# Performance work log

Measured on AMD Instinct MI355X. Metric: run time of the kernel, lower is better.

Reference implementation:

```python
import jax, jax.numpy as jnp
import numpy as np

B, T, A_DIM, Z_DIM, K = 128, 80, 32, 64, 16


def setup_inputs() -> dict:
    key = jax.random.key(0)
    k1, k2, k3, k4 = jax.random.split(key, 4)
    obs = jax.random.normal(k1, (B, T, A_DIM), jnp.float32)
    alpha_logits = jax.random.normal(k2, (B, T, K), jnp.float32)
    # torch init: A = eye(z) repeated K times; small noise keeps 80-step recursion stable
    A_K = jnp.eye(Z_DIM, dtype=jnp.float32)[None] + 0.005 * jax.random.normal(k3, (K, Z_DIM, Z_DIM), jnp.float32)
    # torch init: C = 0.05 * randn
    C_K = 0.05 * jax.random.normal(k4, (K, A_DIM, Z_DIM), jnp.float32)
    return {"obs": obs, "alpha_logits": alpha_logits, "A_K": A_K, "C_K": C_K}


def _kalman(obs, A, C):
    # obs [B,T,a], A [B,T,z,z], C [B,T,a,z]
    Bq, Tq, a_dim = obs.shape
    z_dim = A.shape[-1]
    dt = obs.dtype
    Q = 0.08 * jnp.eye(z_dim, dtype=dt)
    R = 0.03 * jnp.eye(a_dim, dtype=dt)
    I = jnp.eye(z_dim, dtype=dt)

    obs_t = jnp.swapaxes(obs, 0, 1)          # [T,B,a]
    A_t = jnp.swapaxes(A, 0, 1)              # [T,B,z,z]
    C_t = jnp.swapaxes(C, 0, 1)              # [T,B,a,z]
    A_next = jnp.concatenate([A_t[1:], A_t[-1:]], axis=0)  # A[t+1]; last unused

    mu0 = jnp.zeros((Bq, z_dim), dt)
    sig0 = jnp.broadcast_to(20.0 * I, (Bq, z_dim, z_dim))

    def filt_step(carry, inp):
        mu_p, sig_p, mu_prev = carry
        At, Anx, Ct, y = inp
        CtT = jnp.swapaxes(Ct, -1, -2)
        S = Ct @ sig_p @ CtT + R                       # [B,a,a]
        Kg = sig_p @ CtT @ jnp.linalg.inv(S)            # [B,z,a]
        Amu = jnp.einsum('bij,bj->bi', At, mu_prev)     # A_t mu_{t-1}
        err = y - jnp.einsum('bij,bj->bi', Ct, Amu)
        mu_f = Amu + jnp.einsum('bij,bj->bi', Kg, err)
        sig_f = (I - Kg @ Ct) @ sig_p
        mu_pn = jnp.einsum('bij,bj->bi', Anx, mu_f)     # prediction with A_{t+1}
        sig_pn = Anx @ sig_f @ jnp.swapaxes(Anx, -1, -2) + Q
        return (mu_pn, sig_pn, mu_f), (mu_f, sig_f, mu_p, sig_p)

    _, (mu_f, sig_f, mu_p, sig_p) = jax.lax.scan(
        filt_step, (mu0, sig0, mu0), (A_t, A_next, C_t, obs_t))

    def smooth_step(carry, inp):
        mu_s, sig_s = carry
        mf, sf, Anx, mpn, spn = inp
        J = sf @ jnp.swapaxes(Anx, -1, -2) @ jnp.linalg.inv(spn)
        mu = mf + jnp.einsum('bij,bj->bi', J, mu_s - mpn)
        sig = sf + J @ (sig_s - spn) @ jnp.swapaxes(J, -1, -2)
        return (mu, sig), (mu, sig)

    init = (mu_f[-1], sig_f[-1])
    _, (mu_sm, sig_sm) = jax.lax.scan(
        smooth_step, init,
        (mu_f[:-1], sig_f[:-1], A_t[1:], mu_p[1:], sig_p[1:]),
        reverse=True)
    mu_sm = jnp.concatenate([mu_sm, mu_f[-1:]], axis=0)
    sig_sm = jnp.concatenate([sig_sm, sig_f[-1:]], axis=0)
    return jnp.swapaxes(mu_sm, 0, 1), jnp.swapaxes(sig_sm, 0, 1)  # [B,T,z], [B,T,z,z]


def reference(obs, alpha_logits, A_K, C_K):
    w = jax.nn.softmax(alpha_logits, axis=-1)                # [B,T,K]
    A = jnp.einsum('btk,kij->btij', w, A_K)                  # [B,T,z,z]
    C = jnp.einsum('btk,kij->btij', w, C_K)                  # [B,T,a,z]
    return _kalman(obs, A, C)
```

## Files before the change

### kernel.cpp

```cpp
#include <hip/hip_runtime.h>

#define B_ 128
#define T_ 80
#define AD 32
#define ZD 64
#define KD 16
#define S8 68
#define SC 36

__device__ __forceinline__ float4 ld4(const float* p) { return *(const float4*)p; }
__device__ __forceinline__ void st4f(float* p, float4 v) { *(float4*)p = v; }

__device__ __forceinline__ float4 comb4(float4 c, float4 x0, float4 x1, float4 x2, float4 x3) {
    return make_float4(c.x*x0.x + c.y*x1.x + c.z*x2.x + c.w*x3.x,
                       c.x*x0.y + c.y*x1.y + c.z*x2.y + c.w*x3.y,
                       c.x*x0.z + c.y*x1.z + c.z*x2.z + c.w*x3.z,
                       c.x*x0.w + c.y*x1.w + c.z*x2.w + c.w*x3.w);
}

__device__ __forceinline__ void pinv4(float4 q0, float4 q1, float4 q2, float4 q3,
                                      float4& pi0, float4& pi1, float4& pi2, float4& pi3)
{
    const float ra = 1.0f / (q0.x*q1.y - q0.y*q1.x);
    const float ai00 =  q1.y*ra, ai01 = -q0.y*ra, ai10 = -q1.x*ra, ai11 = q0.x*ra;
    const float ca00 = q2.x*ai00 + q2.y*ai10, ca01 = q2.x*ai01 + q2.y*ai11;
    const float ca10 = q3.x*ai00 + q3.y*ai10, ca11 = q3.x*ai01 + q3.y*ai11;
    const float s00 = q2.z - (ca00*q0.z + ca01*q1.z), s01 = q2.w - (ca00*q0.w + ca01*q1.w);
    const float s10 = q3.z - (ca10*q0.z + ca11*q1.z), s11 = q3.w - (ca10*q0.w + ca11*q1.w);
    const float rs = 1.0f / (s00*s11 - s01*s10);
    const float si00 = s11*rs, si01 = -s01*rs, si10 = -s10*rs, si11 = s00*rs;
    const float ab00 = ai00*q0.z + ai01*q1.z, ab01 = ai00*q0.w + ai01*q1.w;
    const float ab10 = ai10*q0.z + ai11*q1.z, ab11 = ai10*q0.w + ai11*q1.w;
    const float t00 = ab00*si00 + ab01*si10, t01 = ab00*si01 + ab01*si11;
    const float t10 = ab10*si00 + ab11*si10, t11 = ab10*si01 + ab11*si11;
    const float tl00 = ai00 + (t00*ca00 + t01*ca10), tl01 = ai01 + (t00*ca01 + t01*ca11);
    const float tl10 = ai10 + (t10*ca00 + t11*ca10), tl11 = ai11 + (t10*ca01 + t11*ca11);
    const float bl00 = -(si00*ca00 + si01*ca10), bl01 = -(si00*ca01 + si01*ca11);
    const float bl10 = -(si10*ca00 + si11*ca10), bl11 = -(si10*ca01 + si11*ca11);
    pi0 = make_float4(tl00, tl01, -t00, -t01);
    pi1 = make_float4(tl10, tl11, -t10, -t11);
    pi2 = make_float4(bl00, bl01, si00, si01);
    pi3 = make_float4(bl10, bl11, si10, si11);
}

template<int KL, int AS, int BS, bool ATRANS>
__device__ __forceinline__ void mm64(const float* __restrict__ Pa, const float* __restrict__ Qb,
                                     float acc[2][4], int r2, int c4)
{
#pragma unroll 8
    for (int k = 0; k < KL; k++) {
        float aA, aB;
        if (ATRANS) { aA = Pa[k * AS + r2];   aB = Pa[k * AS + r2 + 1]; }
        else        { aA = Pa[r2 * AS + k];   aB = Pa[(r2 + 1) * AS + k]; }
        const float4 bv = ld4(&Qb[k * BS + c4]);
        acc[0][0] += aA * bv.x; acc[0][1] += aA * bv.y; acc[0][2] += aA * bv.z; acc[0][3] += aA * bv.w;
        acc[1][0] += aB * bv.x; acc[1][1] += aB * bv.y; acc[1][2] += aB * bv.z; acc[1][3] += aB * bv.w;
    }
}

__global__ __launch_bounds__(512, 2)
void kvae_kernel(const float* __restrict__ obs, const float* __restrict__ logits,
                 const float* __restrict__ AK, const float* __restrict__ CK,
                 float* __restrict__ out)
{
    __shared__ __align__(16) float W[T_ * KD];
    __shared__ __align__(16) float Am[ZD * S8];
    __shared__ __align__(16) float At[ZD * S8];
    __shared__ __align__(16) float SP[ZD * S8];
    __shared__ __align__(16) float SF[ZD * S8];
    __shared__ __align__(16) float Mm[ZD * S8];
    __shared__ __align__(16) float Pool[9984];
    __shared__ __align__(16) float pvL[512];
    __shared__ __align__(16) float pvR[512];
    __shared__ __align__(16) float fbb[512];
    __shared__ __align__(16) float pvE[8];
    __shared__ __align__(16) float y_s[32];
    __shared__ __align__(16) float errv[32];
    __shared__ __align__(16) float uev[32];
    __shared__ __align__(16) float mup[64];
    __shared__ __align__(16) float muf[64];
    __shared__ __align__(16) float mus[64];
    __shared__ __align__(16) float mpn[64];
    __shared__ __align__(16) float dv[64];

    float* T1 = Pool;
    float* CM = Pool + 2176;
    float* CT = Pool + 4352;
    float* U_ = Pool + 6656;
    float* S_ = Pool + 8832;
    float* Xb = Pool;
    float* SG = Pool + 4352;

    const int tid = threadIdx.x;
    const int b   = blockIdx.x;

    const int r16 = tid >> 4;
    const int cg  = tid & 15;
    const int c4  = cg << 2;
    const int c2  = cg << 1;
    const int r2  = r16 << 1;
    const int gi  = tid >> 3;
    const int gs  = tid & 7;

    const float* obs_b = obs    + (size_t)b * T_ * AD;
    const float* lg_b  = logits + (size_t)b * T_ * KD;
    float* omu = out + (size_t)b * T_ * ZD;
    float* osg = out + (size_t)B_ * T_ * ZD + (size_t)b * T_ * ZD * ZD;
    const float4* AK4 = (const float4*)AK;
    const float4* CK4 = (const float4*)CK;

    auto mixA = [&](int tt) {
#pragma unroll
        for (int rr = 0; rr < 2; rr++) {
            const int r = r2 + rr;
            float4 a = make_float4(0.f, 0.f, 0.f, 0.f);
#pragma unroll
            for (int k = 0; k < KD; k++) {
                const float wk = W[tt * KD + k];
                const float4 v = AK4[k * 1024 + r * 16 + cg];
                a.x += wk * v.x; a.y += wk * v.y; a.z += wk * v.z; a.w += wk * v.w;
            }
            st4f(&Am[r * S8 + c4], a);
            At[(c4 + 0) * S8 + r] = a.x; At[(c4 + 1) * S8 + r] = a.y;
            At[(c4 + 2) * S8 + r] = a.z; At[(c4 + 3) * S8 + r] = a.w;
        }
    };
    auto mixC = [&](int tt) {
        float4 a = make_float4(0.f, 0.f, 0.f, 0.f);
#pragma unroll
        for (int k = 0; k < KD; k++) {
            const float wk = W[tt * KD + k];
            const float4 v = CK4[k * 512 + r16 * 16 + cg];
            a.x += wk * v.x; a.y += wk * v.y; a.z += wk * v.z; a.w += wk * v.w;
        }
        st4f(&CM[r16 * S8 + c4], a);
        CT[(c4 + 0) * SC + r16] = a.x; CT[(c4 + 1) * SC + r16] = a.y;
        CT[(c4 + 2) * SC + r16] = a.z; CT[(c4 + 3) * SC + r16] = a.w;
    };

    if (tid < T_) {
        float l[KD]; float mx = -1e30f;
#pragma unroll
        for (int k = 0; k < KD; k++) { l[k] = lg_b[tid * KD + k]; mx = fmaxf(mx, l[k]); }
        float s = 0.f;
#pragma unroll
        for (int k = 0; k < KD; k++) { l[k] = expf(l[k] - mx); s += l[k]; }
        const float inv = 1.0f / s;
#pragma unroll
        for (int k = 0; k < KD; k++) W[tid * KD + k] = l[k] * inv;
    }
#pragma unroll
    for (int rr = 0; rr < 2; rr++) {
        const int r = r2 + rr;
#pragma unroll
        for (int j = 0; j < 4; j++) SP[r * S8 + c4 + j] = (r == c4 + j) ? 20.0f : 0.0f;
    }
    if (tid < ZD) mup[tid] = 0.0f;
    __syncthreads();

    for (int t = 0; t < T_; t++) {
        if (t < T_ - 1) mixA(t + 1);
        mixC(t);
        if (tid < AD) y_s[tid] = obs_b[t * AD + tid];
        __syncthreads();

        {
            float a0 = 0, a1 = 0, a2 = 0, a3 = 0;
            const float* pa = CM + r16 * S8;
#pragma unroll 8
            for (int k = 0; k < ZD; k++) {
                const float a = pa[k];
                const float4 bv = ld4(&SP[k * S8 + c4]);
                a0 += a * bv.x; a1 += a * bv.y; a2 += a * bv.z; a3 += a * bv.w;
            }
            T1[r16 * S8 + c4 + 0] = a0; T1[r16 * S8 + c4 + 1] = a1;
            T1[r16 * S8 + c4 + 2] = a2; T1[r16 * S8 + c4 + 3] = a3;
        }
        __syncthreads();

        {
            float a0 = 0, a1 = 0;
            const float* pa = T1 + r16 * S8;
#pragma unroll 8
            for (int k = 0; k < ZD; k++) {
                const float a = pa[k];
                const float2 bv = *(const float2*)&CT[k * SC + c2];
                a0 += a * bv.x; a1 += a * bv.y;
            }
            if (r16 == c2)     a0 += 0.03f;
            if (r16 == c2 + 1) a1 += 0.03f;
            S_[r16 * SC + c2] = a0; S_[r16 * SC + c2 + 1] = a1;
        }
        if (tid < AD) {
            float s = 0.f;
#pragma unroll
            for (int k4 = 0; k4 < ZD; k4 += 4) {
                const float4 cm = ld4(&CM[tid * S8 + k4]);
                const float4 mu = ld4(&mup[k4]);
                s += cm.x*mu.x + cm.y*mu.y + cm.z*mu.z + cm.w*mu.w;
            }
            errv[tid] = y_s[tid] - s;
        }
        __syncthreads();

        {
            const int hi = r16, hs = cg;
            float4 aL = make_float4(0, 0, 0, 0);
            float4 aR = ld4(&T1[hi * S8 + hs * 4]);
            float e = 0.f;
            if (hs < 8) aL = ld4(&S_[hi * SC + hs * 4]);
            if (hs == 15) e = errv[hi];
            if (hi < 4) {
                if (hs < 8) st4f(&pvL[hi * 32 + hs * 4], aL);
                st4f(&pvR[hi * 64 + hs * 4], aR);
                if (hs == 15) pvE[hi] = e;
            }
            if (hs == 0) st4f(&fbb[hi * 4], aL);
            __syncthreads();

#pragma unroll 2
            for (int j = 0; j < 8; ++j) {
                const int par = j & 1, nb = par ^ 1;
                const bool isp = (hi >> 2) == j;
                const float4 f  = ld4(&fbb[par * 128 + hi * 4]);
                const float4 q0 = ld4(&fbb[par * 128 + (4 * j + 0) * 4]);
                const float4 q1 = ld4(&fbb[par * 128 + (4 * j + 1) * 4]);
                const float4 q2 = ld4(&fbb[par * 128 + (4 * j + 2) * 4]);
                const float4 q3 = ld4(&fbb[par * 128 + (4 * j + 3) * 4]);
                float4 pi0, pi1, pi2, pi3;
                pinv4(q0, q1, q2, q3, pi0, pi1, pi2, pi3);
                const int rr = hi & 3;
                const float4 coef = isp ? (rr == 0 ? pi0 : rr == 1 ? pi1 : rr == 2 ? pi2 : pi3)
                                        : comb4(f, pi0, pi1, pi2, pi3);
                {
                    const float4 x0 = ld4(&pvR[par * 256 + 0 * 64 + hs * 4]);
                    const float4 x1 = ld4(&pvR[par * 256 + 1 * 64 + hs * 4]);
                    const float4 x2 = ld4(&pvR[par * 256 + 2 * 64 + hs * 4]);
                    const float4 x3 = ld4(&pvR[par * 256 + 3 * 64 + hs * 4]);
                    const float4 c = comb4(coef, x0, x1, x2, x3);
                    if (isp) aR = c;
                    else { aR.x -= c.x; aR.y -= c.y; aR.z -= c.z; aR.w -= c.w; }
                }
                if (hs < 8) {
                    const float4 x0 = ld4(&pvL[par * 128 + 0 * 32 + hs * 4]);
                    const float4 x1 = ld4(&pvL[par * 128 + 1 * 32 + hs * 4]);
                    const float4 x2 = ld4(&pvL[par * 128 + 2 * 32 + hs * 4]);
                    const float4 x3 = ld4(&pvL[par * 128 + 3 * 32 + hs * 4]);
                    const float4 c = comb4(coef, x0, x1, x2, x3);
                    if (isp) aL = c;
                    else { aL.x -= c.x; aL.y -= c.y; aL.z -= c.z; aL.w -= c.w; }
                }
                if (hs == 15) {
                    const float e0 = pvE[par * 4 + 0], e1 = pvE[par * 4 + 1];
                    const float e2 = pvE[par * 4 + 2], e3 = pvE[par * 4 + 3];
                    const float ce = coef.x * e0 + coef.y * e1 + coef.z * e2 + coef.w * e3;
                    if (isp) e = ce; else e -= ce;
                }
                if (j < 7) {
                    if ((hi >> 2) == j + 1) {
                        if (hs < 8) st4f(&pvL[nb * 128 + (hi & 3) * 32 + hs * 4], aL);
                        st4f(&pvR[nb * 256 + (hi & 3) * 64 + hs * 4], aR);
                        if (hs == 15) pvE[nb * 4 + (hi & 3)] = e;
                    }
                    if (hs == j + 1) st4f(&fbb[nb * 128 + hi * 4], aL);
                }
                __syncthreads();
            }
            st4f(&U_[hi * S8 + hs * 4], aR);
            if (hs == 15) uev[hi] = e;
        }
        __syncthreads();

        {
            float acc[2][4] = {};
            mm64<AD, S8, S8, true>(T1, U_, acc, r2, c4);
            float* og = osg + (size_t)t * ZD * ZD;
#pragma unroll
            for (int rr = 0; rr < 2; rr++) {
                const int r = r2 + rr;
                const float4 sp = ld4(&SP[r * S8 + c4]);
                const float4 v = make_float4(sp.x - acc[rr][0], sp.y - acc[rr][1],
                                             sp.z - acc[rr][2], sp.w - acc[rr][3]);
                st4f(&SF[r * S8 + c4], v);
                *(float4*)(og + r * ZD + c4) = v;
            }
        }
        if (tid < ZD) {
            float s = 0.f;
#pragma unroll
            for (int k = 0; k < AD; k++) s += T1[k * S8 + tid] * uev[k];
            const float v = mup[tid] + s;
            muf[tid] = v;
            omu[t * ZD + tid] = v;
        }
        __syncthreads();

        if (t < T_ - 1) {
            {
                float acc[2][4] = {};
                mm64<ZD, S8, S8, false>(Am, SF, acc, r2, c4);
#pragma unroll
                for (int rr = 0; rr < 2; rr++)
                    st4f(&Mm[(r2 + rr) * S8 + c4],
                         make_float4(acc[rr][0], acc[rr][1], acc[rr][2], acc[rr][3]));
            }
            __syncthreads();
            {
                float acc[2][4] = {};
                mm64<ZD, S8, S8, false>(Mm, At, acc, r2, c4);
#pragma unroll
                for (int rr = 0; rr < 2; rr++) {
                    const int r = r2 + rr;
#pragma unroll
                    for (int j = 0; j < 4; j++)
                        SP[r * S8 + c4 + j] = acc[rr][j] + ((r == c4 + j) ? 0.08f : 0.0f);
                }
            }
            if (tid >= 448) {
                const int i = tid - 448;
                float s = 0.f;
                const float* pa = Am + i * S8;
#pragma unroll 8
                for (int k = 0; k < ZD; k++) s += pa[k] * muf[k];
                mup[i] = s;
            }
            __syncthreads();
        }
    }

#pragma unroll
    for (int rr = 0; rr < 2; rr++)
        st4f(&SG[(r2 + rr) * S8 + c4], ld4(&SF[(r2 + rr) * S8 + c4]));
    if (tid < ZD) mus[tid] = muf[tid];
    __syncthreads();

    for (int t = T_ - 2; t >= 0; t--) {
        mixA(t + 1);
        {
            const float4* og4 = (const float4*)(osg + (size_t)t * ZD * ZD);
#pragma unroll
            for (int rr = 0; rr < 2; rr++)
                st4f(&SF[(r2 + rr) * S8 + c4], og4[(r2 + rr) * 16 + cg]);
        }
        if (tid >= 448) muf[tid - 448] = omu[t * ZD + (tid - 448)];
        __syncthreads();

        {
            float acc[2][4] = {};
            mm64<ZD, S8, S8, false>(Am, SF, acc, r2, c4);
#pragma unroll
            for (int rr = 0; rr < 2; rr++)
                st4f(&Mm[(r2 + rr) * S8 + c4],
                     make_float4(acc[rr][0], acc[rr][1], acc[rr][2], acc[rr][3]));
        }
        if (tid >= 448) {
            const int i = tid - 448;
            float s = 0.f;
            const float* pa = Am + i * S8;
#pragma unroll 8
            for (int k = 0; k < ZD; k++) s += pa[k] * muf[k];
            mpn[i] = s;
        }
        __syncthreads();

        {
            float acc[2][4] = {};
            mm64<ZD, S8, S8, false>(Mm, At, acc, r2, c4);
#pragma unroll
            for (int rr = 0; rr < 2; rr++) {
                const int r = r2 + rr;
#pragma unroll
                for (int j = 0; j < 4; j++)
                    SP[r * S8 + c4 + j] = acc[rr][j] + ((r == c4 + j) ? 0.08f : 0.0f);
            }
        }
        if (tid >= 448) { const int i = tid - 448; dv[i] = mus[i] - mpn[i]; }
        __syncthreads();

        {
            float4 aL0 = ld4(&SP[gi * S8 + gs * 8]);
            float4 aL1 = ld4(&SP[gi * S8 + gs * 8 + 4]);
            float4 aR0 = ld4(&Mm[gi * S8 + gs * 8]);
            float4 aR1 = ld4(&Mm[gi * S8 + gs * 8 + 4]);
            if (gi < 4) {
                st4f(&pvL[gi * 64 + gs * 8], aL0); st4f(&pvL[gi * 64 + gs * 8 + 4], aL1);
                st4f(&pvR[gi * 64 + gs * 8], aR0); st4f(&pvR[gi * 64 + gs * 8 + 4], aR1);
            }
            if (gs == 0) st4f(&fbb[gi * 4], aL0);
            __syncthreads();

#pragma unroll 2
            for (int j = 0; j < 16; ++j) {
                const int par = j & 1, nb = par ^ 1;
                const bool isp = (gi >> 2) == j;
                const float4 f  = ld4(&fbb[par * 256 + gi * 4]);
                const float4 q0 = ld4(&fbb[par * 256 + (4 * j + 0) * 4]);
                const float4 q1 = ld4(&fbb[par * 256 + (4 * j + 1) * 4]);
                const float4 q2 = ld4(&fbb[par * 256 + (4 * j + 2) * 4]);
                const float4 q3 = ld4(&fbb[par * 256 + (4 * j + 3) * 4]);
                float4 pi0, pi1, pi2, pi3;
                pinv4(q0, q1, q2, q3, pi0, pi1, pi2, pi3);
                const int rr = gi & 3;
                const float4 coef = isp ? (rr == 0 ? pi0 : rr == 1 ? pi1 : rr == 2 ? pi2 : pi3)
                                        : comb4(f, pi0, pi1, pi2, pi3);
                {
                    const float4 x0 = ld4(&pvL[par * 256 + 0 * 64 + gs * 8]);
                    const float4 x1 = ld4(&pvL[par * 256 + 1 * 64 + gs * 8]);
                    const float4 x2 = ld4(&pvL[par * 256 + 2 * 64 + gs * 8]);
                    const float4 x3 = ld4(&pvL[par * 256 + 3 * 64 + gs * 8]);
                    const float4 c = comb4(coef, x0, x1, x2, x3);
                    if (isp) aL0 = c;
                    else { aL0.x -= c.x; aL0.y -= c.y; aL0.z -= c.z; aL0.w -= c.w; }
                }
                {
                    const float4 x0 = ld4(&pvL[par * 256 + 0 * 64 + gs * 8 + 4]);
                    const float4 x1 = ld4(&pvL[par * 256 + 1 * 64 + gs * 8 + 4]);
                    const float4 x2 = ld4(&pvL[par * 256 + 2 * 64 + gs * 8 + 4]);
                    const float4 x3 = ld4(&pvL[par * 256 + 3 * 64 + gs * 8 + 4]);
                    const float4 c = comb4(coef, x0, x1, x2, x3);
                    if (isp) aL1 = c;
                    else { aL1.x -= c.x; aL1.y -= c.y; aL1.z -= c.z; aL1.w -= c.w; }
                }
                {
                    const float4 x0 = ld4(&pvR[par * 256 + 0 * 64 + gs * 8]);
                    const float4 x1 = ld4(&pvR[par * 256 + 1 * 64 + gs * 8]);
                    const float4 x2 = ld4(&pvR[par * 256 + 2 * 64 + gs * 8]);
                    const float4 x3 = ld4(&pvR[par * 256 + 3 * 64 + gs * 8]);
                    const float4 c = comb4(coef, x0, x1, x2, x3);
                    if (isp) aR0 = c;
                    else { aR0.x -= c.x; aR0.y -= c.y; aR0.z -= c.z; aR0.w -= c.w; }
                }
                {
                    const float4 x0 = ld4(&pvR[par * 256 + 0 * 64 + gs * 8 + 4]);
                    const float4 x1 = ld4(&pvR[par * 256 + 1 * 64 + gs * 8 + 4]);
                    const float4 x2 = ld4(&pvR[par * 256 + 2 * 64 + gs * 8 + 4]);
                    const float4 x3 = ld4(&pvR[par * 256 + 3 * 64 + gs * 8 + 4]);
                    const float4 c = comb4(coef, x0, x1, x2, x3);
                    if (isp) aR1 = c;
                    else { aR1.x -= c.x; aR1.y -= c.y; aR1.z -= c.z; aR1.w -= c.w; }
                }
                if (j < 15) {
                    if ((gi >> 2) == j + 1) {
                        const int rn = gi & 3;
                        st4f(&pvL[nb * 256 + rn * 64 + gs * 8], aL0);
                        st4f(&pvL[nb * 256 + rn * 64 + gs * 8 + 4], aL1);
                        st4f(&pvR[nb * 256 + rn * 64 + gs * 8], aR0);
                        st4f(&pvR[nb * 256 + rn * 64 + gs * 8 + 4], aR1);
                    }
                    if (gs == ((j + 1) >> 1))
                        st4f(&fbb[nb * 256 + gi * 4], ((j + 1) & 1) ? aL1 : aL0);
                }
                __syncthreads();
            }
            st4f(&Xb[gi * S8 + gs * 8], aR0);
            st4f(&Xb[gi * S8 + gs * 8 + 4], aR1);
        }
        __syncthreads();

        {
            float acc[2][4] = {};
            mm64<ZD, S8, S8, false>(SG, Xb, acc, r2, c4);
#pragma unroll
            for (int rr = 0; rr < 2; rr++) {
                const int r = r2 + rr;
                const float4 m = ld4(&Mm[r * S8 + c4]);
                SP[r * S8 + c4 + 0] = acc[rr][0] - m.x;
                SP[r * S8 + c4 + 1] = acc[rr][1] - m.y;
                SP[r * S8 + c4 + 2] = acc[rr][2] - m.z;
                SP[r * S8 + c4 + 3] = acc[rr][3] - m.w;
            }
        }
        __syncthreads();

        {
            float acc[2][4] = {};
            mm64<ZD, S8, S8, true>(Xb, SP, acc, r2, c4);
            float* og = osg + (size_t)t * ZD * ZD;
#pragma unroll
            for (int rr = 0; rr < 2; rr++) {
                const int r = r2 + rr;
                const float4 sf = ld4(&SF[r * S8 + c4]);
                const float4 v = make_float4(sf.x + acc[rr][0], sf.y + acc[rr][1],
                                             sf.z + acc[rr][2], sf.w + acc[rr][3]);
                st4f(&SG[r * S8 + c4], v);
                *(float4*)(og + r * ZD + c4) = v;
            }
        }
        if (tid < ZD) {
            float s = 0.f;
#pragma unroll 8
            for (int k = 0; k < ZD; k++) s += Xb[k * S8 + tid] * dv[k];
            const float v = muf[tid] + s;
            mus[tid] = v;
            omu[t * ZD + tid] = v;
        }
        __syncthreads();
    }
}

extern "C" void kernel_launch(void* const* d_in, const int* in_sizes, int n_in,
                              void* d_out, int out_size, void* d_ws, size_t ws_size,
                              hipStream_t stream) {
    const float* obs = (const float*)d_in[0];
    const float* lg  = (const float*)d_in[1];
    const float* AK  = (const float*)d_in[2];
    const float* CK  = (const float*)d_in[3];
    (void)d_ws; (void)ws_size; (void)in_sizes; (void)n_in; (void)out_size;
    kvae_kernel<<<dim3(B_), dim3(512), 0, stream>>>(obs, lg, AK, CK, (float*)d_out);
}
```

Baseline: 3.609 ms.

## Double block size to 1024 threads with one output row-quad per thread

Launches 1024 threads per batch element instead of 512 and remaps every 64x64 matmul so each thread computes one row of four outputs rather than two. The 32x32 innovation covariance and the block Gauss-Jordan eliminations are redistributed across the wider block, and eliminations now skip columns that are already reduced. The aim is to cut the serial per-thread work inside this latency-bound recursion, since only 128 blocks exist on a large GPU. The cost is more threads waiting at each barrier, fewer registers per thread, and an extra barrier where the S computation was split out.

```diff
diff --git a/kernel.cpp b/kernel.cpp
--- a/kernel.cpp
+++ b/kernel.cpp
@@ -10,7 +10,9 @@
 
 __device__ __forceinline__ float4 ld4(const float* p) { return *(const float4*)p; }
 __device__ __forceinline__ void st4f(float* p, float4 v) { *(float4*)p = v; }
-
+__device__ __forceinline__ float4 sub4(float4 a, float4 b) {
+    return make_float4(a.x - b.x, a.y - b.y, a.z - b.z, a.w - b.w);
+}
 __device__ __forceinline__ float4 comb4(float4 c, float4 x0, float4 x1, float4 x2, float4 x3) {
     return make_float4(c.x*x0.x + c.y*x1.x + c.z*x2.x + c.w*x3.x,
                        c.x*x0.y + c.y*x1.y + c.z*x2.y + c.w*x3.y,
@@ -44,21 +46,20 @@
 }
 
 template<int KL, int AS, int BS, bool ATRANS>
-__device__ __forceinline__ void mm64(const float* __restrict__ Pa, const float* __restrict__ Qb,
-                                     float acc[2][4], int r2, int c4)
+__device__ __forceinline__ float4 mm14(const float* __restrict__ Pa, const float* __restrict__ Qb,
+                                       int r, int c4)
 {
+    float a0 = 0.f, a1 = 0.f, a2 = 0.f, a3 = 0.f;
 #pragma unroll 8
     for (int k = 0; k < KL; k++) {
-        float aA, aB;
-        if (ATRANS) { aA = Pa[k * AS + r2];   aB = Pa[k * AS + r2 + 1]; }
-        else        { aA = Pa[r2 * AS + k];   aB = Pa[(r2 + 1) * AS + k]; }
+        const float a = ATRANS ? Pa[k * AS + r] : Pa[r * AS + k];
         const float4 bv = ld4(&Qb[k * BS + c4]);
-        acc[0][0] += aA * bv.x; acc[0][1] += aA * bv.y; acc[0][2] += aA * bv.z; acc[0][3] += aA * bv.w;
-        acc[1][0] += aB * bv.x; acc[1][1] += aB * bv.y; acc[1][2] += aB * bv.z; acc[1][3] += aB * bv.w;
+        a0 += a * bv.x; a1 += a * bv.y; a2 += a * bv.z; a3 += a * bv.w;
     }
-}
-
-__global__ __launch_bounds__(512, 2)
+    return make_float4(a0, a1, a2, a3);
+}
+
+__global__ __launch_bounds__(1024, 4)
 void kvae_kernel(const float* __restrict__ obs, const float* __restrict__ logits,
                  const float* __restrict__ AK, const float* __restrict__ CK,
                  float* __restrict__ out)
@@ -94,13 +95,9 @@
     const int tid = threadIdx.x;
     const int b   = blockIdx.x;
 
-    const int r16 = tid >> 4;
+    const int rw  = tid >> 4;
     const int cg  = tid & 15;
     const int c4  = cg << 2;
-    const int c2  = cg << 1;
-    const int r2  = r16 << 1;
-    const int gi  = tid >> 3;
-    const int gs  = tid & 7;
 
     const float* obs_b = obs    + (size_t)b * T_ * AD;
     const float* lg_b  = logits + (size_t)b * T_ * KD;
@@ -110,32 +107,29 @@
     const float4* CK4 = (const float4*)CK;
 
     auto mixA = [&](int tt) {
-#pragma unroll
-        for (int rr = 0; rr < 2; rr++) {
-            const int r = r2 + rr;
-            float4 a = make_float4(0.f, 0.f, 0.f, 0.f);
-#pragma unroll
-            for (int k = 0; k < KD; k++) {
-                const float wk = W[tt * KD + k];
-                const float4 v = AK4[k * 1024 + r * 16 + cg];
-                a.x += wk * v.x; a.y += wk * v.y; a.z += wk * v.z; a.w += wk * v.w;
-            }
-            st4f(&Am[r * S8 + c4], a);
-            At[(c4 + 0) * S8 + r] = a.x; At[(c4 + 1) * S8 + r] = a.y;
-            At[(c4 + 2) * S8 + r] = a.z; At[(c4 + 3) * S8 + r] = a.w;
-        }
+        float4 a = make_float4(0.f, 0.f, 0.f, 0.f);
+#pragma unroll
+        for (int k = 0; k < KD; k++) {
+            const float wk = W[tt * KD + k];
+            const float4 v = AK4[k * 1024 + rw * 16 + cg];
+            a.x += wk * v.x; a.y += wk * v.y; a.z += wk * v.z; a.w += wk * v.w;
+        }
+        st4f(&Am[rw * S8 + c4], a);
+        At[(c4 + 0) * S8 + rw] = a.x; At[(c4 + 1) * S8 + rw] = a.y;
+        At[(c4 + 2) * S8 + rw] = a.z; At[(c4 + 3) * S8 + rw] = a.w;
     };
     auto mixC = [&](int tt) {
+        const int r = tid >> 4;
         float4 a = make_float4(0.f, 0.f, 0.f, 0.f);
 #pragma unroll
         for (int k = 0; k < KD; k++) {
             const float wk = W[tt * KD + k];
-            const float4 v = CK4[k * 512 + r16 * 16 + cg];
+            const float4 v = CK4[k * 512 + r * 16 + cg];
             a.x += wk * v.x; a.y += wk * v.y; a.z += wk * v.z; a.w += wk * v.w;
         }
-        st4f(&CM[r16 * S8 + c4], a);
-        CT[(c4 + 0) * SC + r16] = a.x; CT[(c4 + 1) * SC + r16] = a.y;
-        CT[(c4 + 2) * SC + r16] = a.z; CT[(c4 + 3) * SC + r16] = a.w;
+        st4f(&CM[r * S8 + c4], a);
+        CT[(c4 + 0) * SC + r] = a.x; CT[(c4 + 1) * SC + r] = a.y;
+        CT[(c4 + 2) * SC + r] = a.z; CT[(c4 + 3) * SC + r] = a.w;
     };
 
     if (tid < T_) {
@@ -150,46 +144,28 @@
         for (int k = 0; k < KD; k++) W[tid * KD + k] = l[k] * inv;
     }
 #pragma unroll
-    for (int rr = 0; rr < 2; rr++) {
-        const int r = r2 + rr;
-#pragma unroll
-        for (int j = 0; j < 4; j++) SP[r * S8 + c4 + j] = (r == c4 + j) ? 20.0f : 0.0f;
-    }
+    for (int j = 0; j < 4; j++) SP[rw * S8 + c4 + j] = (rw == c4 + j) ? 20.0f : 0.0f;
     if (tid < ZD) mup[tid] = 0.0f;
     __syncthreads();
 
     for (int t = 0; t < T_; t++) {
         if (t < T_ - 1) mixA(t + 1);
-        mixC(t);
-        if (tid < AD) y_s[tid] = obs_b[t * AD + tid];
-        __syncthreads();
-
-        {
-            float a0 = 0, a1 = 0, a2 = 0, a3 = 0;
-            const float* pa = CM + r16 * S8;
+        if (tid < 512) mixC(t);
+        if (tid >= 992) y_s[tid - 992] = obs_b[t * AD + (tid - 992)];
+        __syncthreads();
+
+        {
+            const int r = tid >> 5;
+            const int c2 = (tid & 31) << 1;
+            float a0 = 0.f, a1 = 0.f;
+            const float* pa = CM + r * S8;
 #pragma unroll 8
             for (int k = 0; k < ZD; k++) {
                 const float a = pa[k];
-                const float4 bv = ld4(&SP[k * S8 + c4]);
-                a0 += a * bv.x; a1 += a * bv.y; a2 += a * bv.z; a3 += a * bv.w;
-            }
-            T1[r16 * S8 + c4 + 0] = a0; T1[r16 * S8 + c4 + 1] = a1;
-            T1[r16 * S8 + c4 + 2] = a2; T1[r16 * S8 + c4 + 3] = a3;
-        }
-        __syncthreads();
-
-        {
-            float a0 = 0, a1 = 0;
-            const float* pa = T1 + r16 * S8;
-#pragma unroll 8
-            for (int k = 0; k < ZD; k++) {
-                const float a = pa[k];
-                const float2 bv = *(const float2*)&CT[k * SC + c2];
+                const float2 bv = *(const float2*)&SP[k * S8 + c2];
                 a0 += a * bv.x; a1 += a * bv.y;
             }
-            if (r16 == c2)     a0 += 0.03f;
-            if (r16 == c2 + 1) a1 += 0.03f;
-            S_[r16 * SC + c2] = a0; S_[r16 * SC + c2 + 1] = a1;
+            T1[r * S8 + c2] = a0; T1[r * S8 + c2 + 1] = a1;
         }
         if (tid < AD) {
             float s = 0.f;
@@ -204,16 +180,34 @@
         __syncthreads();
 
         {
-            const int hi = r16, hs = cg;
+            const int r = tid >> 5;
+            const int c = tid & 31;
+            float s0 = 0.f, s1 = 0.f;
+            const float* pa = T1 + r * S8;
+            const float* pb = CT + c;
+#pragma unroll 8
+            for (int k = 0; k < ZD; k += 2) {
+                s0 += pa[k] * pb[k * SC];
+                s1 += pa[k + 1] * pb[(k + 1) * SC];
+            }
+            float s = s0 + s1;
+            if (r == c) s += 0.03f;
+            S_[r * SC + c] = s;
+        }
+        __syncthreads();
+
+        {
+            const int hi = tid >> 5, hs = tid & 31;
             float4 aL = make_float4(0, 0, 0, 0);
-            float4 aR = ld4(&T1[hi * S8 + hs * 4]);
+            float4 aR = make_float4(0, 0, 0, 0);
             float e = 0.f;
             if (hs < 8) aL = ld4(&S_[hi * SC + hs * 4]);
-            if (hs == 15) e = errv[hi];
+            else if (hs < 24) aR = ld4(&T1[hi * S8 + (hs - 8) * 4]);
+            else if (hs == 24) e = errv[hi];
             if (hi < 4) {
                 if (hs < 8) st4f(&pvL[hi * 32 + hs * 4], aL);
-                st4f(&pvR[hi * 64 + hs * 4], aR);
-                if (hs == 15) pvE[hi] = e;
+                else if (hs < 24) st4f(&pvR[hi * 64 + (hs - 8) * 4], aR);
+                else if (hs == 24) pvE[hi] = e;
             }
             if (hs == 0) st4f(&fbb[hi * 4], aL);
             __syncthreads();
@@ -221,69 +215,64 @@
 #pragma unroll 2
             for (int j = 0; j < 8; ++j) {
                 const int par = j & 1, nb = par ^ 1;
-                const bool isp = (hi >> 2) == j;
-                const float4 f  = ld4(&fbb[par * 128 + hi * 4]);
-                const float4 q0 = ld4(&fbb[par * 128 + (4 * j + 0) * 4]);
-                const float4 q1 = ld4(&fbb[par * 128 + (4 * j + 1) * 4]);
-                const float4 q2 = ld4(&fbb[par * 128 + (4 * j + 2) * 4]);
-                const float4 q3 = ld4(&fbb[par * 128 + (4 * j + 3) * 4]);
-                float4 pi0, pi1, pi2, pi3;
-                pinv4(q0, q1, q2, q3, pi0, pi1, pi2, pi3);
-                const int rr = hi & 3;
-                const float4 coef = isp ? (rr == 0 ? pi0 : rr == 1 ? pi1 : rr == 2 ? pi2 : pi3)
-                                        : comb4(f, pi0, pi1, pi2, pi3);
-                {
-                    const float4 x0 = ld4(&pvR[par * 256 + 0 * 64 + hs * 4]);
-                    const float4 x1 = ld4(&pvR[par * 256 + 1 * 64 + hs * 4]);
-                    const float4 x2 = ld4(&pvR[par * 256 + 2 * 64 + hs * 4]);
-                    const float4 x3 = ld4(&pvR[par * 256 + 3 * 64 + hs * 4]);
-                    const float4 c = comb4(coef, x0, x1, x2, x3);
-                    if (isp) aR = c;
-                    else { aR.x -= c.x; aR.y -= c.y; aR.z -= c.z; aR.w -= c.w; }
-                }
-                if (hs < 8) {
-                    const float4 x0 = ld4(&pvL[par * 128 + 0 * 32 + hs * 4]);
-                    const float4 x1 = ld4(&pvL[par * 128 + 1 * 32 + hs * 4]);
-                    const float4 x2 = ld4(&pvL[par * 128 + 2 * 32 + hs * 4]);
-                    const float4 x3 = ld4(&pvL[par * 128 + 3 * 32 + hs * 4]);
-                    const float4 c = comb4(coef, x0, x1, x2, x3);
-                    if (isp) aL = c;
-                    else { aL.x -= c.x; aL.y -= c.y; aL.z -= c.z; aL.w -= c.w; }
-                }
-                if (hs == 15) {
-                    const float e0 = pvE[par * 4 + 0], e1 = pvE[par * 4 + 1];
-                    const float e2 = pvE[par * 4 + 2], e3 = pvE[par * 4 + 3];
-                    const float ce = coef.x * e0 + coef.y * e1 + coef.z * e2 + coef.w * e3;
-                    if (isp) e = ce; else e -= ce;
-                }
-                if (j < 7) {
-                    if ((hi >> 2) == j + 1) {
-                        if (hs < 8) st4f(&pvL[nb * 128 + (hi & 3) * 32 + hs * 4], aL);
-                        st4f(&pvR[nb * 256 + (hi & 3) * 64 + hs * 4], aR);
-                        if (hs == 15) pvE[nb * 4 + (hi & 3)] = e;
+                if (hs <= 24) {
+                    const bool isp = (hi >> 2) == j;
+                    const int i4 = hi & 3;
+                    const float4 q0 = ld4(&fbb[par * 128 + (4 * j + 0) * 4]);
+                    const float4 q1 = ld4(&fbb[par * 128 + (4 * j + 1) * 4]);
+                    const float4 q2 = ld4(&fbb[par * 128 + (4 * j + 2) * 4]);
+                    const float4 q3 = ld4(&fbb[par * 128 + (4 * j + 3) * 4]);
+                    float4 pi0, pi1, pi2, pi3;
+                    pinv4(q0, q1, q2, q3, pi0, pi1, pi2, pi3);
+                    float4 coef;
+                    if (isp) coef = (i4 == 0 ? pi0 : i4 == 1 ? pi1 : i4 == 2 ? pi2 : pi3);
+                    else {
+                        const float4 f = ld4(&fbb[par * 128 + hi * 4]);
+                        coef = comb4(f, pi0, pi1, pi2, pi3);
                     }
-                    if (hs == j + 1) st4f(&fbb[nb * 128 + hi * 4], aL);
+                    if (hs < 8) {
+                        if (hs > j - 1) {
+                            const float4 c = comb4(coef,
+                                ld4(&pvL[par * 256 + 0 * 32 + hs * 4]),
+                                ld4(&pvL[par * 256 + 1 * 32 + hs * 4]),
+                                ld4(&pvL[par * 256 + 2 * 32 + hs * 4]),
+                                ld4(&pvL[par * 256 + 3 * 32 + hs * 4]));
+                            if (isp) aL = c; else aL = sub4(aL, c);
+                        }
+                    } else if (hs < 24) {
+                        const float4 c = comb4(coef,
+                            ld4(&pvR[par * 256 + 0 * 64 + (hs - 8) * 4]),
+                            ld4(&pvR[par * 256 + 1 * 64 + (hs - 8) * 4]),
+                            ld4(&pvR[par * 256 + 2 * 64 + (hs - 8) * 4]),
+                            ld4(&pvR[par * 256 + 3 * 64 + (hs - 8) * 4]));
+                        if (isp) aR = c; else aR = sub4(aR, c);
+                    } else {
+                        const float4 ev = ld4(&pvE[par * 4]);
+                        const float ce = coef.x*ev.x + coef.y*ev.y + coef.z*ev.z + coef.w*ev.w;
+                        if (isp) e = ce; else e -= ce;
+                    }
+                    if (j < 7) {
+                        if ((hi >> 2) == j + 1) {
+                            if (hs < 8) { if (hs > j) st4f(&pvL[nb * 256 + i4 * 32 + hs * 4], aL); }
+                            else if (hs < 24) st4f(&pvR[nb * 256 + i4 * 64 + (hs - 8) * 4], aR);
+                            else pvE[nb * 4 + i4] = e;
+                        }
+                        if (hs == j + 1) st4f(&fbb[nb * 128 + hi * 4], aL);
+                    }
                 }
                 __syncthreads();
             }
-            st4f(&U_[hi * S8 + hs * 4], aR);
-            if (hs == 15) uev[hi] = e;
-        }
-        __syncthreads();
-
-        {
-            float acc[2][4] = {};
-            mm64<AD, S8, S8, true>(T1, U_, acc, r2, c4);
-            float* og = osg + (size_t)t * ZD * ZD;
-#pragma unroll
-            for (int rr = 0; rr < 2; rr++) {
-                const int r = r2 + rr;
-                const float4 sp = ld4(&SP[r * S8 + c4]);
-                const float4 v = make_float4(sp.x - acc[rr][0], sp.y - acc[rr][1],
-                                             sp.z - acc[rr][2], sp.w - acc[rr][3]);
-                st4f(&SF[r * S8 + c4], v);
-                *(float4*)(og + r * ZD + c4) = v;
-            }
+            if (hs >= 8 && hs < 24) st4f(&U_[hi * S8 + (hs - 8) * 4], aR);
+            else if (hs == 24) uev[hi] = e;
+        }
+        __syncthreads();
+
+        {
+            const float4 acc = mm14<AD, S8, S8, true>(T1, U_, rw, c4);
+            const float4 sp = ld4(&SP[rw * S8 + c4]);
+            const float4 v = make_float4(sp.x - acc.x, sp.y - acc.y, sp.z - acc.z, sp.w - acc.w);
+            st4f(&SF[rw * S8 + c4], v);
+            *(float4*)(osg + (size_t)t * ZD * ZD + rw * ZD + c4) = v;
         }
         if (tid < ZD) {
             float s = 0.f;
@@ -296,195 +285,136 @@
         __syncthreads();
 
         if (t < T_ - 1) {
-            {
-                float acc[2][4] = {};
-                mm64<ZD, S8, S8, false>(Am, SF, acc, r2, c4);
-#pragma unroll
-                for (int rr = 0; rr < 2; rr++)
-                    st4f(&Mm[(r2 + rr) * S8 + c4],
-                         make_float4(acc[rr][0], acc[rr][1], acc[rr][2], acc[rr][3]));
-            }
+            st4f(&Mm[rw * S8 + c4], mm14<ZD, S8, S8, false>(Am, SF, rw, c4));
             __syncthreads();
             {
-                float acc[2][4] = {};
-                mm64<ZD, S8, S8, false>(Mm, At, acc, r2, c4);
-#pragma unroll
-                for (int rr = 0; rr < 2; rr++) {
-                    const int r = r2 + rr;
-#pragma unroll
-                    for (int j = 0; j < 4; j++)
-                        SP[r * S8 + c4 + j] = acc[rr][j] + ((r == c4 + j) ? 0.08f : 0.0f);
-                }
-            }
-            if (tid >= 448) {
-                const int i = tid - 448;
+                const float4 acc = mm14<ZD, S8, S8, false>(Mm, At, rw, c4);
+                SP[rw * S8 + c4 + 0] = acc.x + ((rw == c4 + 0) ? 0.08f : 0.0f);
+                SP[rw * S8 + c4 + 1] = acc.y + ((rw == c4 + 1) ? 0.08f : 0.0f);
+                SP[rw * S8 + c4 + 2] = acc.z + ((rw == c4 + 2) ? 0.08f : 0.0f);
+                SP[rw * S8 + c4 + 3] = acc.w + ((rw == c4 + 3) ? 0.08f : 0.0f);
+            }
+            if (tid >= 960) {
+                const int i = tid - 960;
                 float s = 0.f;
-                const float* pa = Am + i * S8;
-#pragma unroll 8
-                for (int k = 0; k < ZD; k++) s += pa[k] * muf[k];
+#pragma unroll
+                for (int k4 = 0; k4 < ZD; k4 += 4) {
+                    const float4 am = ld4(&Am[i * S8 + k4]);
+                    const float4 mf = ld4(&muf[k4]);
+                    s += am.x*mf.x + am.y*mf.y + am.z*mf.z + am.w*mf.w;
+                }
                 mup[i] = s;
             }
             __syncthreads();
         }
     }
 
-#pragma unroll
-    for (int rr = 0; rr < 2; rr++)
-        st4f(&SG[(r2 + rr) * S8 + c4], ld4(&SF[(r2 + rr) * S8 + c4]));
+    st4f(&SG[rw * S8 + c4], ld4(&SF[rw * S8 + c4]));
     if (tid < ZD) mus[tid] = muf[tid];
     __syncthreads();
 
     for (int t = T_ - 2; t >= 0; t--) {
         mixA(t + 1);
-        {
-            const float4* og4 = (const float4*)(osg + (size_t)t * ZD * ZD);
-#pragma unroll
-            for (int rr = 0; rr < 2; rr++)
-                st4f(&SF[(r2 + rr) * S8 + c4], og4[(r2 + rr) * 16 + cg]);
-        }
-        if (tid >= 448) muf[tid - 448] = omu[t * ZD + (tid - 448)];
-        __syncthreads();
-
-        {
-            float acc[2][4] = {};
-            mm64<ZD, S8, S8, false>(Am, SF, acc, r2, c4);
-#pragma unroll
-            for (int rr = 0; rr < 2; rr++)
-                st4f(&Mm[(r2 + rr) * S8 + c4],
-                     make_float4(acc[rr][0], acc[rr][1], acc[rr][2], acc[rr][3]));
-        }
-        if (tid >= 448) {
-            const int i = tid - 448;
+        st4f(&SF[rw * S8 + c4],
+             *(const float4*)(osg + (size_t)t * ZD * ZD + rw * ZD + c4));
+        if (tid >= 960) muf[tid - 960] = omu[t * ZD + (tid - 960)];
+        __syncthreads();
+
+        st4f(&Mm[rw * S8 + c4], mm14<ZD, S8, S8, false>(Am, SF, rw, c4));
+        if (tid >= 960) {
+            const int i = tid - 960;
             float s = 0.f;
-            const float* pa = Am + i * S8;
-#pragma unroll 8
-            for (int k = 0; k < ZD; k++) s += pa[k] * muf[k];
+#pragma unroll
+            for (int k4 = 0; k4 < ZD; k4 += 4) {
+                const float4 am = ld4(&Am[i * S8 + k4]);
+                const float4 mf = ld4(&muf[k4]);
+                s += am.x*mf.x + am.y*mf.y + am.z*mf.z + am.w*mf.w;
+            }
             mpn[i] = s;
         }
         __syncthreads();
 
         {
-            float acc[2][4] = {};
-            mm64<ZD, S8, S8, false>(Mm, At, acc, r2, c4);
-#pragma unroll
-            for (int rr = 0; rr < 2; rr++) {
-                const int r = r2 + rr;
-#pragma unroll
-                for (int j = 0; j < 4; j++)
-                    SP[r * S8 + c4 + j] = acc[rr][j] + ((r == c4 + j) ? 0.08f : 0.0f);
-            }
-        }
-        if (tid >= 448) { const int i = tid - 448; dv[i] = mus[i] - mpn[i]; }
-        __syncthreads();
-
-        {
-            float4 aL0 = ld4(&SP[gi * S8 + gs * 8]);
-            float4 aL1 = ld4(&SP[gi * S8 + gs * 8 + 4]);
-            float4 aR0 = ld4(&Mm[gi * S8 + gs * 8]);
-            float4 aR1 = ld4(&Mm[gi * S8 + gs * 8 + 4]);
+            const float4 acc = mm14<ZD, S8, S8, false>(Mm, At, rw, c4);
+            SP[rw * S8 + c4 + 0] = acc.x + ((rw == c4 + 0) ? 0.08f : 0.0f);
+            SP[rw * S8 + c4 + 1] = acc.y + ((rw == c4 + 1) ? 0.08f : 0.0f);
+            SP[rw * S8 + c4 + 2] = acc.z + ((rw == c4 + 2) ? 0.08f : 0.0f);
+            SP[rw * S8 + c4 + 3] = acc.w + ((rw == c4 + 3) ? 0.08f : 0.0f);
+        }
+        if (tid >= 960) { const int i = tid - 960; dv[i] = mus[i] - mpn[i]; }
+        __syncthreads();
+
+        {
+            const int gi = tid >> 4, gs = tid & 15;
+            float4 aL = ld4(&SP[gi * S8 + gs * 4]);
+            float4 aR = ld4(&Mm[gi * S8 + gs * 4]);
             if (gi < 4) {
-                st4f(&pvL[gi * 64 + gs * 8], aL0); st4f(&pvL[gi * 64 + gs * 8 + 4], aL1);
-                st4f(&pvR[gi * 64 + gs * 8], aR0); st4f(&pvR[gi * 64 + gs * 8 + 4], aR1);
-            }
-            if (gs == 0) st4f(&fbb[gi * 4], aL0);
+                st4f(&pvL[gi * 64 + gs * 4], aL);
+                st4f(&pvR[gi * 64 + gs * 4], aR);
+            }
+            if (gs == 0) st4f(&fbb[gi * 4], aL);
             __syncthreads();
 
 #pragma unroll 2
             for (int j = 0; j < 16; ++j) {
                 const int par = j & 1, nb = par ^ 1;
                 const bool isp = (gi >> 2) == j;
-                const float4 f  = ld4(&fbb[par * 256 + gi * 4]);
+                const int i4 = gi & 3;
                 const float4 q0 = ld4(&fbb[par * 256 + (4 * j + 0) * 4]);
                 const float4 q1 = ld4(&fbb[par * 256 + (4 * j + 1) * 4]);
                 const float4 q2 = ld4(&fbb[par * 256 + (4 * j + 2) * 4]);
                 const float4 q3 = ld4(&fbb[par * 256 + (4 * j + 3) * 4]);
                 float4 pi0, pi1, pi2, pi3;
                 pinv4(q0, q1, q2, q3, pi0, pi1, pi2, pi3);
-                const int rr = gi & 3;
-                const float4 coef = isp ? (rr == 0 ? pi0 : rr == 1 ? pi1 : rr == 2 ? pi2 : pi3)
-                                        : comb4(f, pi0, pi1, pi2, pi3);
+                float4 coef;
+                if (isp) coef = (i4 == 0 ? pi0 : i4 == 1 ? pi1 : i4 == 2 ? pi2 : pi3);
+                else {
+                    const float4 f = ld4(&fbb[par * 256 + gi * 4]);
+                    coef = comb4(f, pi0, pi1, pi2, pi3);
+                }
                 {
-                    const float4 x0 = ld4(&pvL[par * 256 + 0 * 64 + gs * 8]);
-                    const float4 x1 = ld4(&pvL[par * 256 + 1 * 64 + gs * 8]);
-                    const float4 x2 = ld4(&pvL[par * 256 + 2 * 64 + gs * 8]);
-                    const float4 x3 = ld4(&pvL[par * 256 + 3 * 64 + gs * 8]);
-                    const float4 c = comb4(coef, x0, x1, x2, x3);
-                    if (isp) aL0 = c;
-                    else { aL0.x -= c.x; aL0.y -= c.y; aL0.z -= c.z; aL0.w -= c.w; }
-                }
-                {
-                    const float4 x0 = ld4(&pvL[par * 256 + 0 * 64 + gs * 8 + 4]);
-                    const float4 x1 = ld4(&pvL[par * 256 + 1 * 64 + gs * 8 + 4]);
-                    const float4 x2 = ld4(&pvL[par * 256 + 2 * 64 + gs * 8 + 4]);
-                    const float4 x3 = ld4(&pvL[par * 256 + 3 * 64 + gs * 8 + 4]);
-                    const float4 c = comb4(coef, x0, x1, x2, x3);
-                    if (isp) aL1 = c;
-                    else { aL1.x -= c.x; aL1.y -= c.y; aL1.z -= c.z; aL1.w -= c.w; }
-                }
-                {
-                    const float4 x0 = ld4(&pvR[par * 256 + 0 * 64 + gs * 8]);
-                    const float4 x1 = ld4(&pvR[par * 256 + 1 * 64 + gs * 8]);
-                    const float4 x2 = ld4(&pvR[par * 256 + 2 * 64 + gs * 8]);
-                    const float4 x3 = ld4(&pvR[par * 256 + 3 * 64 + gs * 8]);
-                    const float4 c = comb4(coef, x0, x1, x2, x3);
-                    if (isp) aR0 = c;
-                    else { aR0.x -= c.x; aR0.y -= c.y; aR0.z -= c.z; aR0.w -= c.w; }
-                }
-                {
-                    const float4 x0 = ld4(&pvR[par * 256 + 0 * 64 + gs * 8 + 4]);
-                    const float4 x1 = ld4(&pvR[par * 256 + 1 * 64 + gs * 8 + 4]);
-                    const float4 x2 = ld4(&pvR[par * 256 + 2 * 64 + gs * 8 + 4]);
-                    const float4 x3 = ld4(&pvR[par * 256 + 3 * 64 + gs * 8 + 4]);
-                    const float4 c = comb4(coef, x0, x1, x2, x3);
-                    if (isp) aR1 = c;
-                    else { aR1.x -= c.x; aR1.y -= c.y; aR1.z -= c.z; aR1.w -= c.w; }
+                    const float4 c = comb4(coef,
+                        ld4(&pvR[par * 256 + 0 * 64 + gs * 4]),
+                        ld4(&pvR[par * 256 + 1 * 64 + gs * 4]),
+                        ld4(&pvR[par * 256 + 2 * 64 + gs * 4]),
+                        ld4(&pvR[par * 256 + 3 * 64 + gs * 4]));
+                    if (isp) aR = c; else aR = sub4(aR, c);
+                }
+                if (gs > j - 1) {
+                    const float4 c = comb4(coef,
+                        ld4(&pvL[par * 256 + 0 * 64 + gs * 4]),
+                        ld4(&pvL[par * 256 + 1 * 64 + gs * 4]),
+                        ld4(&pvL[par * 256 + 2 * 64 + gs * 4]),
+                        ld4(&pvL[par * 256 + 3 * 64 + gs * 4]));
+                    if (isp) aL = c; else aL = sub4(aL, c);
                 }
                 if (j < 15) {
                     if ((gi >> 2) == j + 1) {
-                        const int rn = gi & 3;
-                        st4f(&pvL[nb * 256 + rn * 64 + gs * 8], aL0);
-                        st4f(&pvL[nb * 256 + rn * 64 + gs * 8 + 4], aL1);
-                        st4f(&pvR[nb * 256 + rn * 64 + gs * 8], aR0);
-                        st4f(&pvR[nb * 256 + rn * 64 + gs * 8 + 4], aR1);
+                        st4f(&pvR[nb * 256 + i4 * 64 + gs * 4], aR);
+                        if (gs > j) st4f(&pvL[nb * 256 + i4 * 64 + gs * 4], aL);
                     }
-                    if (gs == ((j + 1) >> 1))
-                        st4f(&fbb[nb * 256 + gi * 4], ((j + 1) & 1) ? aL1 : aL0);
+                    if (gs == j + 1) st4f(&fbb[nb * 256 + gi * 4], aL);
                 }
                 __syncthreads();
             }
-            st4f(&Xb[gi * S8 + gs * 8], aR0);
-            st4f(&Xb[gi * S8 + gs * 8 + 4], aR1);
-        }
-        __syncthreads();
-
-        {
-            float acc[2][4] = {};
-            mm64<ZD, S8, S8, false>(SG, Xb, acc, r2, c4);
-#pragma unroll
-            for (int rr = 0; rr < 2; rr++) {
-                const int r = r2 + rr;
-                const float4 m = ld4(&Mm[r * S8 + c4]);
-                SP[r * S8 + c4 + 0] = acc[rr][0] - m.x;
-                SP[r * S8 + c4 + 1] = acc[rr][1] - m.y;
-                SP[r * S8 + c4 + 2] = acc[rr][2] - m.z;
-                SP[r * S8 + c4 + 3] = acc[rr][3] - m.w;
-            }
-        }
-        __syncthreads();
-
-        {
-            float acc[2][4] = {};
-            mm64<ZD, S8, S8, true>(Xb, SP, acc, r2, c4);
-            float* og = osg + (size_t)t * ZD * ZD;
-#pragma unroll
-            for (int rr = 0; rr < 2; rr++) {
-                const int r = r2 + rr;
-                const float4 sf = ld4(&SF[r * S8 + c4]);
-                const float4 v = make_float4(sf.x + acc[rr][0], sf.y + acc[rr][1],
-                                             sf.z + acc[rr][2], sf.w + acc[rr][3]);
-                st4f(&SG[r * S8 + c4], v);
-                *(float4*)(og + r * ZD + c4) = v;
-            }
+            st4f(&Xb[gi * S8 + gs * 4], aR);
+        }
+        __syncthreads();
+
+        {
+            const float4 acc = mm14<ZD, S8, S8, false>(SG, Xb, rw, c4);
+            const float4 m = ld4(&Mm[rw * S8 + c4]);
+            st4f(&SP[rw * S8 + c4],
+                 make_float4(acc.x - m.x, acc.y - m.y, acc.z - m.z, acc.w - m.w));
+        }
+        __syncthreads();
+
+        {
+            const float4 acc = mm14<ZD, S8, S8, true>(Xb, SP, rw, c4);
+            const float4 sf = ld4(&SF[rw * S8 + c4]);
+            const float4 v = make_float4(sf.x + acc.x, sf.y + acc.y, sf.z + acc.z, sf.w + acc.w);
+            st4f(&SG[rw * S8 + c4], v);
+            *(float4*)(osg + (size_t)t * ZD * ZD + rw * ZD + c4) = v;
         }
         if (tid < ZD) {
             float s = 0.f;
@@ -506,5 +436,5 @@
     const float* AK  = (const float*)d_in[2];
     const float* CK  = (const float*)d_in[3];
     (void)d_ws; (void)ws_size; (void)in_sizes; (void)n_in; (void)out_size;
-    kvae_kernel<<<dim3(B_), dim3(512), 0, stream>>>(obs, lg, AK, CK, (float*)d_out);
-}
+    kvae_kernel<<<dim3(B_), dim3(1024), 0, stream>>>(obs, lg, AK, CK, (float*)d_out);
+}
```

New measurement: 5.210 ms. 1.44x slower.
